# Optimization experiments

Measured on AMD Instinct MI355X. Metric: run time of the kernel, lower is better.

Reference implementation:

```python
import jax, jax.numpy as jnp
import numpy as np

N = 50000      # nodes
E = 800000     # edges (before self-loops)
NFEAT = 128
NHID = 32
H = 8
NCLASS = 47
NEG_SLOPE = 0.2  # PyG GATv2Conv default


def gatv2_layer(x, src, dst, Wl, Wr, att, b, n):
    """One GATv2Conv layer (concat over heads). att: [H, C]."""
    h, c = att.shape
    xl = (x @ Wl).reshape(n, h, c)  # source transform (lin_l)
    xr = (x @ Wr).reshape(n, h, c)  # target transform (lin_r)
    e = jax.nn.leaky_relu(xl[src] + xr[dst], NEG_SLOPE)   # [E, H, C]
    logits = jnp.einsum('ehc,hc->eh', e, att)             # [E, H]
    # segment softmax over incoming edges of each target node
    m = jax.ops.segment_max(logits, dst, num_segments=n)  # [N, H]
    alpha = jnp.exp(logits - m[dst])
    denom = jax.ops.segment_sum(alpha, dst, num_segments=n)
    alpha = alpha / (denom[dst] + 1e-16)
    msg = xl[src] * alpha[:, :, None]                     # [E, H, C]
    out = jax.ops.segment_sum(msg, dst, num_segments=n)   # [N, H, C]
    return out.reshape(n, h * c) + b


def setup_inputs():
    key = jax.random.key(0)
    ks = jax.random.split(key, 16)
    s = 0.1
    x = jax.random.normal(ks[0], (N, NFEAT), jnp.float32)
    edge_index = jax.random.randint(ks[1], (2, E), 0, N)
    HID = H * NHID  # 256
    params = dict(
        Wl0=jax.random.normal(ks[2], (NFEAT, HID), jnp.float32) * s,
        Wr0=jax.random.normal(ks[3], (NFEAT, HID), jnp.float32) * s,
        a0=jax.random.normal(ks[4], (H, NHID), jnp.float32) * s,
        b0=jnp.zeros((HID,), jnp.float32),
        Wl1=jax.random.normal(ks[5], (HID, HID), jnp.float32) * s,
        Wr1=jax.random.normal(ks[6], (HID, HID), jnp.float32) * s,
        a1=jax.random.normal(ks[7], (H, NHID), jnp.float32) * s,
        b1=jnp.zeros((HID,), jnp.float32),
        Wl2=jax.random.normal(ks[8], (HID, NCLASS), jnp.float32) * s,
        Wr2=jax.random.normal(ks[9], (HID, NCLASS), jnp.float32) * s,
        a2=jax.random.normal(ks[10], (1, NCLASS), jnp.float32) * s,
        b2=jnp.zeros((NCLASS,), jnp.float32),
    )
    return {"x": x, "edge_index": edge_index, **params}


def reference(x, edge_index, Wl0, Wr0, a0, b0, Wl1, Wr1, a1, b1, Wl2, Wr2, a2, b2):
    n = x.shape[0]
    # PyG GATv2Conv adds self-loops by default
    loops = jnp.arange(n, dtype=edge_index.dtype)
    src = jnp.concatenate([edge_index[0], loops])
    dst = jnp.concatenate([edge_index[1], loops])
    h = gatv2_layer(x, src, dst, Wl0, Wr0, a0, b0, n)
    h = jax.nn.elu(h)
    h = gatv2_layer(h, src, dst, Wl1, Wr1, a1, b1, n)
    h = jax.nn.elu(h)
    h = gatv2_layer(h, src, dst, Wl2, Wr2, a2, b2, n)
    return jax.nn.log_softmax(h, axis=-1)
```

## Files before the change

### kernel.cpp

```cpp
#include <hip/hip_runtime.h>
#include <cmath>


#define NFEAT 128
#define HID 256
#define NCLS 47
#define L2PAD 64

typedef __attribute__((ext_vector_type(8))) short bf16x8;
typedef __attribute__((ext_vector_type(4))) float f32x4;

__device__ __forceinline__ unsigned short f2b(float f) {
  unsigned int u = __builtin_bit_cast(unsigned int, f);
  u += 0x7FFFu + ((u >> 16) & 1u);
  return (unsigned short)(u >> 16);
}
__device__ __forceinline__ float b2f(unsigned short s) {
  return __builtin_bit_cast(float, (unsigned int)s << 16);
}
__device__ __forceinline__ float b2f_lo(unsigned int u) {
  return __builtin_bit_cast(float, u << 16);
}
__device__ __forceinline__ float b2f_hi(unsigned int u) {
  return __builtin_bit_cast(float, u & 0xFFFF0000u);
}

__device__ __forceinline__ float group8_sum(float v) {
  v += __shfl_xor(v, 1, 64);
  v += __shfl_xor(v, 2, 64);
  v += __shfl_xor(v, 4, 64);
  return v;
}

__global__ void k_cast_bf16(const float* __restrict__ in,
                            unsigned short* __restrict__ out, int n4) {
  int i = blockIdx.x * blockDim.x + threadIdx.x;
  if (i < n4) {
    float4 v = reinterpret_cast<const float4*>(in)[i];
    ushort4 o = {f2b(v.x), f2b(v.y), f2b(v.z), f2b(v.w)};
    reinterpret_cast<ushort4*>(out)[i] = o;
  }
}

__global__ void k_wt(const float* __restrict__ W, unsigned short* __restrict__ WT,
                     int K, int M, int Mpad) {
  int i = blockIdx.x * blockDim.x + threadIdx.x;
  if (i >= Mpad * K) return;
  int m = i / K, k = i - m * K;
  WT[i] = (m < M) ? f2b(W[(size_t)k * M + m]) : 0;
}

__global__ void k_init_deg(int* __restrict__ deg, int n) {
  int i = blockIdx.x * blockDim.x + threadIdx.x;
  if (i < n) deg[i] = 1;
}

__global__ void k_count(const int* __restrict__ dst, int* __restrict__ deg, int e) {
  int i = blockIdx.x * blockDim.x + threadIdx.x;
  if (i < e) atomicAdd(&deg[dst[i]], 1);
}

__global__ __launch_bounds__(256) void k_bsum(const int* __restrict__ deg,
                                              int* __restrict__ bsum, int n) {
  int t = threadIdx.x;
  int base = blockIdx.x * 1024 + t * 4;
  int s = 0;
  if (base + 3 < n) {
    int4 v = *reinterpret_cast<const int4*>(deg + base);
    s = v.x + v.y + v.z + v.w;
  } else {
    for (int j = 0; j < 4; ++j) { int i = base + j; if (i < n) s += deg[i]; }
  }
  #pragma unroll
  for (int off = 1; off < 64; off <<= 1) s += __shfl_xor(s, off, 64);
  __shared__ int wsum[4];
  if ((t & 63) == 0) wsum[t >> 6] = s;
  __syncthreads();
  if (t == 0) bsum[blockIdx.x] = wsum[0] + wsum[1] + wsum[2] + wsum[3];
}

__global__ void k_scanb(int* __restrict__ bsum, int nb) {
  int lane = threadIdx.x;
  int v = (lane < nb) ? bsum[lane] : 0;
  #pragma unroll
  for (int off = 1; off < 64; off <<= 1) {
    int u = __shfl_up(v, off, 64);
    if (lane >= off) v += u;
  }
  if (lane < nb) bsum[lane] = v;
}

__global__ __launch_bounds__(256) void k_scanfinal(const int* __restrict__ deg,
                                                   const int* __restrict__ bscan,
                                                   int* __restrict__ rowptr, int n) {
  int t = threadIdx.x, b = blockIdx.x;
  int base = b * 1024 + t * 4;
  int v0 = 0, v1 = 0, v2 = 0, v3 = 0;
  if (base + 3 < n) {
    int4 v = *reinterpret_cast<const int4*>(deg + base);
    v0 = v.x; v1 = v.y; v2 = v.z; v3 = v.w;
  } else {
    if (base < n) v0 = deg[base];
    if (base + 1 < n) v1 = deg[base + 1];
    if (base + 2 < n) v2 = deg[base + 2];
    if (base + 3 < n) v3 = deg[base + 3];
  }
  int s = v0 + v1 + v2 + v3;
  int incl = s;
  #pragma unroll
  for (int off = 1; off < 64; off <<= 1) {
    int u = __shfl_up(incl, off, 64);
    if ((t & 63) >= off) incl += u;
  }
  __shared__ int wsum[4];
  int w = t >> 6, l = t & 63;
  if (l == 63) wsum[w] = incl;
  __syncthreads();
  int woff = 0;
  for (int j = 0; j < w; ++j) woff += wsum[j];
  int excl = incl - s + woff;
  int boff = (b == 0) ? 0 : bscan[b - 1];
  int p = boff + excl;
  if (base < n)     rowptr[base + 1] = p + v0;
  if (base + 1 < n) rowptr[base + 2] = p + v0 + v1;
  if (base + 2 < n) rowptr[base + 3] = p + v0 + v1 + v2;
  if (base + 3 < n) rowptr[base + 4] = p + v0 + v1 + v2 + v3;
  if (b == 0 && t == 0) rowptr[0] = 0;
}

__global__ void k_init_csr(const int* __restrict__ rowptr, int* __restrict__ adj,
                           int* __restrict__ cursor, int n) {
  int i = blockIdx.x * blockDim.x + threadIdx.x;
  if (i < n) { int p = rowptr[i]; adj[p] = i; cursor[i] = p + 1; }
}

__global__ void k_scatter(const int* __restrict__ src, const int* __restrict__ dst,
                          int* __restrict__ cursor, int* __restrict__ adj, int e) {
  int i = blockIdx.x * blockDim.x + threadIdx.x;
  if (i < e) { int p = atomicAdd(&cursor[dst[i]], 1); adj[p] = src[i]; }
}

__global__ __launch_bounds__(256) void gemm_dual_bf16(
    const unsigned short* __restrict__ X, const unsigned short* __restrict__ WlT,
    const unsigned short* __restrict__ WrT, unsigned short* __restrict__ XL,
    unsigned short* __restrict__ XR, int N, int K, int Mpad) {
  __shared__ __align__(16) unsigned short Xs[64][72];
  __shared__ __align__(16) unsigned short Ls[64][72];
  __shared__ __align__(16) unsigned short Rs[64][72];

  const int t = threadIdx.x;
  const int row0 = blockIdx.x * 64;
  const int col0 = blockIdx.y * 64;
  const int w = t >> 6, lane = t & 63;
  const int r15 = lane & 15, kc = lane >> 4;

  f32x4 accL[4], accR[4];
  #pragma unroll
  for (int i = 0; i < 4; ++i) {
    accL[i] = (f32x4){0.f, 0.f, 0.f, 0.f};
    accR[i] = (f32x4){0.f, 0.f, 0.f, 0.f};
  }

  for (int k0 = 0; k0 < K; k0 += 64) {
    #pragma unroll
    for (int cc = 0; cc < 2; ++cc) {
      int c = t + cc * 256;
      int row = c >> 3, seg = (c & 7) * 8;
      int grow = row0 + row;
      if (grow < N) {
        *reinterpret_cast<uint4*>(&Xs[row][seg]) =
            *reinterpret_cast<const uint4*>(X + (size_t)grow * K + k0 + seg);
      } else {
        *reinterpret_cast<uint4*>(&Xs[row][seg]) = (uint4){0, 0, 0, 0};
      }
      *reinterpret_cast<uint4*>(&Ls[row][seg]) =
          *reinterpret_cast<const uint4*>(WlT + (size_t)(col0 + row) * K + k0 + seg);
      *reinterpret_cast<uint4*>(&Rs[row][seg]) =
          *reinterpret_cast<const uint4*>(WrT + (size_t)(col0 + row) * K + k0 + seg);
    }
    __syncthreads();

    #pragma unroll
    for (int ks = 0; ks < 2; ++ks) {
      const bf16x8 a = *reinterpret_cast<const bf16x8*>(&Xs[16 * w + r15][ks * 32 + kc * 8]);
      #pragma unroll
      for (int nf = 0; nf < 4; ++nf) {
        const bf16x8 bl = *reinterpret_cast<const bf16x8*>(&Ls[nf * 16 + r15][ks * 32 + kc * 8]);
        const bf16x8 br = *reinterpret_cast<const bf16x8*>(&Rs[nf * 16 + r15][ks * 32 + kc * 8]);
        accL[nf] = __builtin_amdgcn_mfma_f32_16x16x32_bf16(a, bl, accL[nf], 0, 0, 0);
        accR[nf] = __builtin_amdgcn_mfma_f32_16x16x32_bf16(a, br, accR[nf], 0, 0, 0);
      }
    }
    __syncthreads();
  }

  #pragma unroll
  for (int nf = 0; nf < 4; ++nf) {
    int cc = col0 + nf * 16 + r15;
    #pragma unroll
    for (int i = 0; i < 4; ++i) {
      int rr = row0 + 16 * w + kc * 4 + i;
      if (rr < N) {
        XL[(size_t)rr * Mpad + cc] = f2b(accL[nf][i]);
        XR[(size_t)rr * Mpad + cc] = f2b(accR[nf][i]);
      }
    }
  }
}

__global__ __launch_bounds__(256) void gat_node_hc(
    const unsigned short* __restrict__ xl, const unsigned short* __restrict__ xr,
    const float* __restrict__ att, const float* __restrict__ bias,
    const int* __restrict__ rowptr, const int* __restrict__ adj,
    unsigned short* __restrict__ out, int n) {
  int wid = (blockIdx.x * blockDim.x + threadIdx.x) >> 6;
  int lane = threadIdx.x & 63;
  if (wid >= n) return;

  uint2 pr = *reinterpret_cast<const uint2*>(xr + (size_t)wid * HID + lane * 4);
  const float xr0 = b2f_lo(pr.x), xr1 = b2f_hi(pr.x);
  const float xr2 = b2f_lo(pr.y), xr3 = b2f_hi(pr.y);
  const float4 a = *reinterpret_cast<const float4*>(att + lane * 4);

  float m = -INFINITY, denom = 0.f;
  float a0 = 0.f, a1 = 0.f, a2 = 0.f, a3 = 0.f;

#define EDGE_PREP(p, x0, x1, x2, x3, part)                                 \
  x0 = b2f_lo(p.x); x1 = b2f_hi(p.x); x2 = b2f_lo(p.y); x3 = b2f_hi(p.y);  \
  {                                                                        \
    float t0 = x0 + xr0, t1 = x1 + xr1, t2 = x2 + xr2, t3 = x3 + xr3;      \
    t0 = fmaxf(t0, 0.2f * t0); t1 = fmaxf(t1, 0.2f * t1);                  \
    t2 = fmaxf(t2, 0.2f * t2); t3 = fmaxf(t3, 0.2f * t3);                  \
    part = t0 * a.x + t1 * a.y + t2 * a.z + t3 * a.w;                      \
    part = group8_sum(part);                                               \
  }

#define SLOW_UPDATE(part, x0, x1, x2, x3)                                  \
  {                                                                        \
    float mn = fmaxf(m, part);                                             \
    float so = __expf(m - mn);                                             \
    float wn = __expf(part - mn);                                          \
    denom = denom * so + wn;                                               \
    a0 = a0 * so + wn * x0; a1 = a1 * so + wn * x1;                        \
    a2 = a2 * so + wn * x2; a3 = a3 * so + wn * x3;                        \
    m = mn;                                                                \
  }

  const int beg = rowptr[wid], end = rowptr[wid + 1];
  int i = beg;
  for (; i + 1 < end; i += 2) {
    int u0 = adj[i], u1 = adj[i + 1];
    uint2 p0 = *reinterpret_cast<const uint2*>(xl + (size_t)u0 * HID + lane * 4);
    uint2 p1 = *reinterpret_cast<const uint2*>(xl + (size_t)u1 * HID + lane * 4);
    float x00, x01, x02, x03, part0;
    float x10, x11, x12, x13, part1;
    EDGE_PREP(p0, x00, x01, x02, x03, part0);
    EDGE_PREP(p1, x10, x11, x12, x13, part1);
    float mx = fmaxf(part0, part1);
    if (__any(mx > m + 8.f)) {
      SLOW_UPDATE(part0, x00, x01, x02, x03);
      SLOW_UPDATE(part1, x10, x11, x12, x13);
    } else {
      float w0 = __expf(part0 - m), w1 = __expf(part1 - m);
      denom += w0 + w1;
      a0 += w0 * x00 + w1 * x10; a1 += w0 * x01 + w1 * x11;
      a2 += w0 * x02 + w1 * x12; a3 += w0 * x03 + w1 * x13;
    }
  }
  if (i < end) {
    int u0 = adj[i];
    uint2 p0 = *reinterpret_cast<const uint2*>(xl + (size_t)u0 * HID + lane * 4);
    float x00, x01, x02, x03, part0;
    EDGE_PREP(p0, x00, x01, x02, x03, part0);
    if (__any(part0 > m + 8.f)) {
      SLOW_UPDATE(part0, x00, x01, x02, x03);
    } else {
      float w0 = __expf(part0 - m);
      denom += w0;
      a0 += w0 * x00; a1 += w0 * x01; a2 += w0 * x02; a3 += w0 * x03;
    }
  }
#undef EDGE_PREP
#undef SLOW_UPDATE

  const float inv = 1.f / (denom + 1e-16f);
  const float4 bv = *reinterpret_cast<const float4*>(bias + lane * 4);
  float o[4] = {a0 * inv + bv.x, a1 * inv + bv.y, a2 * inv + bv.z, a3 * inv + bv.w};
  #pragma unroll
  for (int j = 0; j < 4; ++j) o[j] = o[j] > 0.f ? o[j] : (__expf(o[j]) - 1.f);
  ushort4 ov = {f2b(o[0]), f2b(o[1]), f2b(o[2]), f2b(o[3])};
  *reinterpret_cast<ushort4*>(out + (size_t)wid * HID + lane * 4) = ov;
}

__global__ __launch_bounds__(256) void gat_node_l2(
    const unsigned short* __restrict__ xl, const unsigned short* __restrict__ xr,
    const float* __restrict__ att, const float* __restrict__ bias,
    const int* __restrict__ rowptr, const int* __restrict__ adj,
    float* __restrict__ out, int n) {
  int wid = (blockIdx.x * blockDim.x + threadIdx.x) >> 6;
  int lane = threadIdx.x & 63;
  if (wid >= n) return;
  const bool act = lane < NCLS;

  const float xrv = act ? b2f(xr[(size_t)wid * L2PAD + lane]) : 0.f;
  const float a = act ? att[lane] : 0.f;

  float m = -INFINITY, denom = 0.f, acc = 0.f;

#define L2_PREP(u, xv, part)                                               \
  xv = act ? b2f(xl[(size_t)(u) * L2PAD + lane]) : 0.f;                    \
  {                                                                        \
    float e = xv + xrv; e = fmaxf(e, 0.2f * e);                            \
    part = e * a;                                                          \
    _Pragma("unroll")                                                      \
    for (int off = 1; off < 64; off <<= 1) part += __shfl_xor(part, off, 64); \
  }

#define L2_SLOW(part, xv)                                                  \
  {                                                                        \
    float mn = fmaxf(m, part);                                             \
    float so = __expf(m - mn);                                             \
    float wn = __expf(part - mn);                                          \
    denom = denom * so + wn;                                               \
    acc = acc * so + wn * xv;                                              \
    m = mn;                                                                \
  }

  const int beg = rowptr[wid], end = rowptr[wid + 1];
  int i = beg;
  for (; i + 1 < end; i += 2) {
    int u0 = adj[i], u1 = adj[i + 1];
    float xv0, part0, xv1, part1;
    L2_PREP(u0, xv0, part0);
    L2_PREP(u1, xv1, part1);
    float mx = fmaxf(part0, part1);
    if (mx > m + 8.f) {
      L2_SLOW(part0, xv0);
      L2_SLOW(part1, xv1);
    } else {
      float w0 = __expf(part0 - m), w1 = __expf(part1 - m);
      denom += w0 + w1;
      acc += w0 * xv0 + w1 * xv1;
    }
  }
  if (i < end) {
    int u0 = adj[i];
    float xv0, part0;
    L2_PREP(u0, xv0, part0);
    if (part0 > m + 8.f) {
      L2_SLOW(part0, xv0);
    } else {
      float w0 = __expf(part0 - m);
      denom += w0;
      acc += w0 * xv0;
    }
  }
#undef L2_PREP
#undef L2_SLOW

  float r = acc / (denom + 1e-16f) + (act ? bias[lane] : 0.f);
  float rm = act ? r : -INFINITY;
  #pragma unroll
  for (int off = 1; off < 64; off <<= 1) rm = fmaxf(rm, __shfl_xor(rm, off, 64));
  float se = act ? __expf(r - rm) : 0.f;
  #pragma unroll
  for (int off = 1; off < 64; off <<= 1) se += __shfl_xor(se, off, 64);
  if (act) out[(size_t)wid * NCLS + lane] = r - rm - __logf(se);
}

extern "C" void kernel_launch(void* const* d_in, const int* in_sizes, int n_in,
                              void* d_out, int out_size, void* d_ws, size_t ws_size,
                              hipStream_t stream) {
  const float* x   = (const float*)d_in[0];
  const int* ei    = (const int*)d_in[1];
  const float* Wl0 = (const float*)d_in[2];
  const float* Wr0 = (const float*)d_in[3];
  const float* a0  = (const float*)d_in[4];
  const float* b0  = (const float*)d_in[5];
  const float* Wl1 = (const float*)d_in[6];
  const float* Wr1 = (const float*)d_in[7];
  const float* a1  = (const float*)d_in[8];
  const float* b1  = (const float*)d_in[9];
  const float* Wl2 = (const float*)d_in[10];
  const float* Wr2 = (const float*)d_in[11];
  const float* a2  = (const float*)d_in[12];
  const float* b2  = (const float*)d_in[13];

  const int N = in_sizes[0] / NFEAT;
  const int E = in_sizes[1] / 2;
  const int* src = ei;
  const int* dst = ei + E;

  char* ws = (char*)d_ws;
  unsigned short* xlb = (unsigned short*)ws; ws += (size_t)N * HID * 2;
  unsigned short* xrb = (unsigned short*)ws; ws += (size_t)N * HID * 2;
  unsigned short* xb  = (unsigned short*)ws; ws += (size_t)N * NFEAT * 2;
  unsigned short* hb  = (unsigned short*)ws; ws += (size_t)N * HID * 2;
  unsigned short* hb2 = (unsigned short*)ws; ws += (size_t)N * HID * 2;
  unsigned short* WT  = (unsigned short*)ws; ws += (size_t)6 * HID * HID * 2;
  int* deg    = (int*)ws; ws += (size_t)N * sizeof(int);
  int* rowptr = (int*)ws; ws += (size_t)(N + 8) * sizeof(int);
  int* bsum   = (int*)ws; ws += (size_t)64 * sizeof(int);
  int* adj    = (int*)ws; ws += (size_t)(E + N) * sizeof(int);

  unsigned short* WlT0 = WT + 0 * HID * HID;
  unsigned short* WrT0 = WT + 1 * HID * HID;
  unsigned short* WlT1 = WT + 2 * HID * HID;
  unsigned short* WrT1 = WT + 3 * HID * HID;
  unsigned short* WlT2 = WT + 4 * HID * HID;
  unsigned short* WrT2 = WT + 5 * HID * HID;

  const int TB = 256;
  const int nbScan = (N + 1023) / 1024;

  k_cast_bf16<<<(N * NFEAT / 4 + TB - 1) / TB, TB, 0, stream>>>(x, xb, N * NFEAT / 4);
  k_wt<<<(HID * NFEAT + TB - 1) / TB, TB, 0, stream>>>(Wl0, WlT0, NFEAT, HID, HID);
  k_wt<<<(HID * NFEAT + TB - 1) / TB, TB, 0, stream>>>(Wr0, WrT0, NFEAT, HID, HID);
  k_wt<<<(HID * HID + TB - 1) / TB, TB, 0, stream>>>(Wl1, WlT1, HID, HID, HID);
  k_wt<<<(HID * HID + TB - 1) / TB, TB, 0, stream>>>(Wr1, WrT1, HID, HID, HID);
  k_wt<<<(L2PAD * HID + TB - 1) / TB, TB, 0, stream>>>(Wl2, WlT2, HID, NCLS, L2PAD);
  k_wt<<<(L2PAD * HID + TB - 1) / TB, TB, 0, stream>>>(Wr2, WrT2, HID, NCLS, L2PAD);

  k_init_deg<<<(N + TB - 1) / TB, TB, 0, stream>>>(deg, N);
  k_count<<<(E + TB - 1) / TB, TB, 0, stream>>>(dst, deg, E);
  k_bsum<<<nbScan, TB, 0, stream>>>(deg, bsum, N);
  k_scanb<<<1, 64, 0, stream>>>(bsum, nbScan);
  k_scanfinal<<<nbScan, TB, 0, stream>>>(deg, bsum, rowptr, N);
  k_init_csr<<<(N + TB - 1) / TB, TB, 0, stream>>>(rowptr, adj, deg, N);
  k_scatter<<<(E + TB - 1) / TB, TB, 0, stream>>>(src, dst, deg, adj, E);

  const int nodeBlocks = (N + 3) / 4;
  const int rowBlocks = (N + 63) / 64;

  {
    dim3 g(rowBlocks, HID / 64);
    gemm_dual_bf16<<<g, 256, 0, stream>>>(xb, WlT0, WrT0, xlb, xrb, N, NFEAT, HID);
    gat_node_hc<<<nodeBlocks, 256, 0, stream>>>(xlb, xrb, a0, b0, rowptr, adj, hb, N);
  }
  {
    dim3 g(rowBlocks, HID / 64);
    gemm_dual_bf16<<<g, 256, 0, stream>>>(hb, WlT1, WrT1, xlb, xrb, N, HID, HID);
    gat_node_hc<<<nodeBlocks, 256, 0, stream>>>(xlb, xrb, a1, b1, rowptr, adj, hb2, N);
  }
  {
    dim3 g(rowBlocks, 1);
    gemm_dual_bf16<<<g, 256, 0, stream>>>(hb2, WlT2, WrT2, xlb, xrb, N, HID, L2PAD);
    gat_node_l2<<<nodeBlocks, 256, 0, stream>>>(xlb, xrb, a2, b2, rowptr, adj,
                                                (float*)d_out, N);
  }
}
```

Baseline: 451.0 us.

## Split wave across two edges per step and precompute layer-2 edge logits

The hidden-layer aggregation kernel now has each wave's two 32-lane halves process different edges, each loading 8 bf16 features per lane. It keeps per-half online-softmax state and merges the halves at the end, which halves the shuffle-reduction depth and doubles the bytes per load. For the output layer, a new per-edge kernel computes all attention logits up front using a stored destination array. The node kernel then takes a plain max and does exp-weighted sums without per-edge 64-lane reductions. This costs extra work in CSR construction (a vdst array) plus an additional logit buffer pass, and it reuses xb as the layer-2 input buffer.

```diff
diff --git a/kernel.cpp b/kernel.cpp
--- a/kernel.cpp
+++ b/kernel.cpp
@@ -9,6 +9,7 @@
 
 typedef __attribute__((ext_vector_type(8))) short bf16x8;
 typedef __attribute__((ext_vector_type(4))) float f32x4;
+typedef __attribute__((ext_vector_type(2))) float f32x2;
 
 __device__ __forceinline__ unsigned short f2b(float f) {
   unsigned int u = __builtin_bit_cast(unsigned int, f);
@@ -18,18 +19,9 @@
 __device__ __forceinline__ float b2f(unsigned short s) {
   return __builtin_bit_cast(float, (unsigned int)s << 16);
 }
-__device__ __forceinline__ float b2f_lo(unsigned int u) {
-  return __builtin_bit_cast(float, u << 16);
-}
-__device__ __forceinline__ float b2f_hi(unsigned int u) {
-  return __builtin_bit_cast(float, u & 0xFFFF0000u);
-}
-
-__device__ __forceinline__ float group8_sum(float v) {
-  v += __shfl_xor(v, 1, 64);
-  v += __shfl_xor(v, 2, 64);
-  v += __shfl_xor(v, 4, 64);
-  return v;
+__device__ __forceinline__ f32x2 b2f2(unsigned int u) {
+  return (f32x2){__builtin_bit_cast(float, u << 16),
+                 __builtin_bit_cast(float, u & 0xFFFF0000u)};
 }
 
 __global__ void k_cast_bf16(const float* __restrict__ in,
@@ -48,6 +40,11 @@
   if (i >= Mpad * K) return;
   int m = i / K, k = i - m * K;
   WT[i] = (m < M) ? f2b(W[(size_t)k * M + m]) : 0;
+}
+
+__global__ void k_pad_att(const float* __restrict__ a, float* __restrict__ out48) {
+  int i = threadIdx.x;
+  if (i < 48) out48[i] = (i < NCLS) ? a[i] : 0.f;
 }
 
 __global__ void k_init_deg(int* __restrict__ deg, int n) {
@@ -129,15 +126,21 @@
 }
 
 __global__ void k_init_csr(const int* __restrict__ rowptr, int* __restrict__ adj,
-                           int* __restrict__ cursor, int n) {
-  int i = blockIdx.x * blockDim.x + threadIdx.x;
-  if (i < n) { int p = rowptr[i]; adj[p] = i; cursor[i] = p + 1; }
+                           int* __restrict__ vdst, int* __restrict__ cursor, int n) {
+  int i = blockIdx.x * blockDim.x + threadIdx.x;
+  if (i < n) { int p = rowptr[i]; adj[p] = i; vdst[p] = i; cursor[i] = p + 1; }
 }
 
 __global__ void k_scatter(const int* __restrict__ src, const int* __restrict__ dst,
-                          int* __restrict__ cursor, int* __restrict__ adj, int e) {
-  int i = blockIdx.x * blockDim.x + threadIdx.x;
-  if (i < e) { int p = atomicAdd(&cursor[dst[i]], 1); adj[p] = src[i]; }
+                          int* __restrict__ cursor, int* __restrict__ adj,
+                          int* __restrict__ vdst, int e) {
+  int i = blockIdx.x * blockDim.x + threadIdx.x;
+  if (i < e) {
+    int d = dst[i];
+    int p = atomicAdd(&cursor[d], 1);
+    adj[p] = src[i];
+    vdst[p] = d;
+  }
 }
 
 __global__ __launch_bounds__(256) void gemm_dual_bf16(
@@ -216,150 +219,147 @@
   int wid = (blockIdx.x * blockDim.x + threadIdx.x) >> 6;
   int lane = threadIdx.x & 63;
   if (wid >= n) return;
-
-  uint2 pr = *reinterpret_cast<const uint2*>(xr + (size_t)wid * HID + lane * 4);
-  const float xr0 = b2f_lo(pr.x), xr1 = b2f_hi(pr.x);
-  const float xr2 = b2f_lo(pr.y), xr3 = b2f_hi(pr.y);
-  const float4 a = *reinterpret_cast<const float4*>(att + lane * 4);
-
-  float m = -INFINITY, denom = 0.f;
-  float a0 = 0.f, a1 = 0.f, a2 = 0.f, a3 = 0.f;
-
-#define EDGE_PREP(p, x0, x1, x2, x3, part)                                 \
-  x0 = b2f_lo(p.x); x1 = b2f_hi(p.x); x2 = b2f_lo(p.y); x3 = b2f_hi(p.y);  \
-  {                                                                        \
-    float t0 = x0 + xr0, t1 = x1 + xr1, t2 = x2 + xr2, t3 = x3 + xr3;      \
-    t0 = fmaxf(t0, 0.2f * t0); t1 = fmaxf(t1, 0.2f * t1);                  \
-    t2 = fmaxf(t2, 0.2f * t2); t3 = fmaxf(t3, 0.2f * t3);                  \
-    part = t0 * a.x + t1 * a.y + t2 * a.z + t3 * a.w;                      \
-    part = group8_sum(part);                                               \
-  }
-
-#define SLOW_UPDATE(part, x0, x1, x2, x3)                                  \
-  {                                                                        \
-    float mn = fmaxf(m, part);                                             \
-    float so = __expf(m - mn);                                             \
-    float wn = __expf(part - mn);                                          \
-    denom = denom * so + wn;                                               \
-    a0 = a0 * so + wn * x0; a1 = a1 * so + wn * x1;                        \
-    a2 = a2 * so + wn * x2; a3 = a3 * so + wn * x3;                        \
-    m = mn;                                                                \
-  }
+  const int q = lane & 31, half = lane >> 5;
+
+  const uint4 xrp = *reinterpret_cast<const uint4*>(xr + (size_t)wid * HID + q * 8);
+  const f32x2 xr2[4] = {b2f2(xrp.x), b2f2(xrp.y), b2f2(xrp.z), b2f2(xrp.w)};
+  const float4 af0 = *reinterpret_cast<const float4*>(att + q * 8);
+  const float4 af1 = *reinterpret_cast<const float4*>(att + q * 8 + 4);
+  const f32x2 a2[4] = {{af0.x, af0.y}, {af0.z, af0.w},
+                       {af1.x, af1.y}, {af1.z, af1.w}};
+
+  float m = -1e30f, denom = 0.f;
+  f32x2 acc[4] = {{0.f, 0.f}, {0.f, 0.f}, {0.f, 0.f}, {0.f, 0.f}};
 
   const int beg = rowptr[wid], end = rowptr[wid + 1];
-  int i = beg;
-  for (; i + 1 < end; i += 2) {
-    int u0 = adj[i], u1 = adj[i + 1];
-    uint2 p0 = *reinterpret_cast<const uint2*>(xl + (size_t)u0 * HID + lane * 4);
-    uint2 p1 = *reinterpret_cast<const uint2*>(xl + (size_t)u1 * HID + lane * 4);
-    float x00, x01, x02, x03, part0;
-    float x10, x11, x12, x13, part1;
-    EDGE_PREP(p0, x00, x01, x02, x03, part0);
-    EDGE_PREP(p1, x10, x11, x12, x13, part1);
-    float mx = fmaxf(part0, part1);
-    if (__any(mx > m + 8.f)) {
-      SLOW_UPDATE(part0, x00, x01, x02, x03);
-      SLOW_UPDATE(part1, x10, x11, x12, x13);
+  for (int base = beg; base < end; base += 2) {
+    const int i = base + half;
+    const bool act = i < end;
+    const int u = adj[act ? i : base];
+    const uint4 p = *reinterpret_cast<const uint4*>(xl + (size_t)u * HID + q * 8);
+    const f32x2 x2[4] = {b2f2(p.x), b2f2(p.y), b2f2(p.z), b2f2(p.w)};
+    f32x2 s2 = x2[0] * 0.f;
+    #pragma unroll
+    for (int j = 0; j < 4; ++j) {
+      f32x2 z = x2[j] + xr2[j];
+      f32x2 lz = 0.2f * z;
+      f32x2 r = {fmaxf(z.x, lz.x), fmaxf(z.y, lz.y)};
+      s2 += r * a2[j];
+    }
+    float part = s2.x + s2.y;
+    part += __shfl_xor(part, 1, 64);
+    part += __shfl_xor(part, 2, 64);
+    if (!act) part = -1e30f;
+    if (__any(part > m + 8.f)) {
+      float mn = fmaxf(m, part);
+      float so = __expf(m - mn);
+      float wn = act ? __expf(part - mn) : 0.f;
+      denom = denom * so + wn;
+      #pragma unroll
+      for (int j = 0; j < 4; ++j) acc[j] = acc[j] * so + wn * x2[j];
+      m = mn;
     } else {
-      float w0 = __expf(part0 - m), w1 = __expf(part1 - m);
-      denom += w0 + w1;
-      a0 += w0 * x00 + w1 * x10; a1 += w0 * x01 + w1 * x11;
-      a2 += w0 * x02 + w1 * x12; a3 += w0 * x03 + w1 * x13;
-    }
-  }
-  if (i < end) {
-    int u0 = adj[i];
-    uint2 p0 = *reinterpret_cast<const uint2*>(xl + (size_t)u0 * HID + lane * 4);
-    float x00, x01, x02, x03, part0;
-    EDGE_PREP(p0, x00, x01, x02, x03, part0);
-    if (__any(part0 > m + 8.f)) {
-      SLOW_UPDATE(part0, x00, x01, x02, x03);
-    } else {
-      float w0 = __expf(part0 - m);
-      denom += w0;
-      a0 += w0 * x00; a1 += w0 * x01; a2 += w0 * x02; a3 += w0 * x03;
-    }
-  }
-#undef EDGE_PREP
-#undef SLOW_UPDATE
-
-  const float inv = 1.f / (denom + 1e-16f);
-  const float4 bv = *reinterpret_cast<const float4*>(bias + lane * 4);
-  float o[4] = {a0 * inv + bv.x, a1 * inv + bv.y, a2 * inv + bv.z, a3 * inv + bv.w};
-  #pragma unroll
-  for (int j = 0; j < 4; ++j) o[j] = o[j] > 0.f ? o[j] : (__expf(o[j]) - 1.f);
-  ushort4 ov = {f2b(o[0]), f2b(o[1]), f2b(o[2]), f2b(o[3])};
-  *reinterpret_cast<ushort4*>(out + (size_t)wid * HID + lane * 4) = ov;
+      float wn = act ? __expf(part - m) : 0.f;
+      denom += wn;
+      #pragma unroll
+      for (int j = 0; j < 4; ++j) acc[j] += wn * x2[j];
+    }
+  }
+
+  float mo = __shfl_xor(m, 32, 64);
+  float ms = fmaxf(m, mo);
+  float sc = __expf(m - ms);
+  denom *= sc;
+  denom += __shfl_xor(denom, 32, 64);
+  #pragma unroll
+  for (int j = 0; j < 4; ++j) {
+    acc[j] *= sc;
+    acc[j].x += __shfl_xor(acc[j].x, 32, 64);
+    acc[j].y += __shfl_xor(acc[j].y, 32, 64);
+  }
+
+  if (half == 0) {
+    const float inv = 1.f / (denom + 1e-16f);
+    const float4 bf0 = *reinterpret_cast<const float4*>(bias + q * 8);
+    const float4 bf1 = *reinterpret_cast<const float4*>(bias + q * 8 + 4);
+    float o[8] = {acc[0].x * inv + bf0.x, acc[0].y * inv + bf0.y,
+                  acc[1].x * inv + bf0.z, acc[1].y * inv + bf0.w,
+                  acc[2].x * inv + bf1.x, acc[2].y * inv + bf1.y,
+                  acc[3].x * inv + bf1.z, acc[3].y * inv + bf1.w};
+    #pragma unroll
+    for (int j = 0; j < 8; ++j) o[j] = o[j] > 0.f ? o[j] : (__expf(o[j]) - 1.f);
+    uint4 ov;
+    ov.x = (unsigned)f2b(o[0]) | ((unsigned)f2b(o[1]) << 16);
+    ov.y = (unsigned)f2b(o[2]) | ((unsigned)f2b(o[3]) << 16);
+    ov.z = (unsigned)f2b(o[4]) | ((unsigned)f2b(o[5]) << 16);
+    ov.w = (unsigned)f2b(o[6]) | ((unsigned)f2b(o[7]) << 16);
+    *reinterpret_cast<uint4*>(out + (size_t)wid * HID + q * 8) = ov;
+  }
+}
+
+__global__ __launch_bounds__(256) void k_logit_l2(
+    const unsigned short* __restrict__ xl, const unsigned short* __restrict__ xr,
+    const float* __restrict__ att48, const int* __restrict__ adj,
+    const int* __restrict__ vdst, float* __restrict__ logit, int total) {
+  int i = blockIdx.x * blockDim.x + threadIdx.x;
+  if (i >= total) return;
+  const int u = adj[i], v = vdst[i];
+  const uint4* pu = reinterpret_cast<const uint4*>(xl + (size_t)u * L2PAD);
+  const uint4* pv = reinterpret_cast<const uint4*>(xr + (size_t)v * L2PAD);
+  f32x2 s2 = {0.f, 0.f};
+  #pragma unroll
+  for (int b = 0; b < 6; ++b) {
+    const uint4 xu = pu[b], xv = pv[b];
+    const f32x2* a2 = reinterpret_cast<const f32x2*>(att48 + b * 8);
+    const unsigned ua[4] = {xu.x, xu.y, xu.z, xu.w};
+    const unsigned va[4] = {xv.x, xv.y, xv.z, xv.w};
+    #pragma unroll
+    for (int j = 0; j < 4; ++j) {
+      f32x2 z = b2f2(ua[j]) + b2f2(va[j]);
+      f32x2 lz = 0.2f * z;
+      f32x2 r = {fmaxf(z.x, lz.x), fmaxf(z.y, lz.y)};
+      s2 += r * a2[j];
+    }
+  }
+  logit[i] = s2.x + s2.y;
 }
 
 __global__ __launch_bounds__(256) void gat_node_l2(
-    const unsigned short* __restrict__ xl, const unsigned short* __restrict__ xr,
-    const float* __restrict__ att, const float* __restrict__ bias,
-    const int* __restrict__ rowptr, const int* __restrict__ adj,
-    float* __restrict__ out, int n) {
+    const unsigned short* __restrict__ xl, const float* __restrict__ logit,
+    const float* __restrict__ bias, const int* __restrict__ rowptr,
+    const int* __restrict__ adj, float* __restrict__ out, int n) {
   int wid = (blockIdx.x * blockDim.x + threadIdx.x) >> 6;
   int lane = threadIdx.x & 63;
   if (wid >= n) return;
   const bool act = lane < NCLS;
-
-  const float xrv = act ? b2f(xr[(size_t)wid * L2PAD + lane]) : 0.f;
-  const float a = act ? att[lane] : 0.f;
-
-  float m = -INFINITY, denom = 0.f, acc = 0.f;
-
-#define L2_PREP(u, xv, part)                                               \
-  xv = act ? b2f(xl[(size_t)(u) * L2PAD + lane]) : 0.f;                    \
-  {                                                                        \
-    float e = xv + xrv; e = fmaxf(e, 0.2f * e);                            \
-    part = e * a;                                                          \
-    _Pragma("unroll")                                                      \
-    for (int off = 1; off < 64; off <<= 1) part += __shfl_xor(part, off, 64); \
-  }
-
-#define L2_SLOW(part, xv)                                                  \
-  {                                                                        \
-    float mn = fmaxf(m, part);                                             \
-    float so = __expf(m - mn);                                             \
-    float wn = __expf(part - mn);                                          \
-    denom = denom * so + wn;                                               \
-    acc = acc * so + wn * xv;                                              \
-    m = mn;                                                                \
-  }
-
   const int beg = rowptr[wid], end = rowptr[wid + 1];
+
+  float mx = -1e30f;
+  for (int i = beg + lane; i < end; i += 64) mx = fmaxf(mx, logit[i]);
+  #pragma unroll
+  for (int off = 1; off < 64; off <<= 1) mx = fmaxf(mx, __shfl_xor(mx, off, 64));
+
+  float denom = 0.f, acc = 0.f;
   int i = beg;
   for (; i + 1 < end; i += 2) {
     int u0 = adj[i], u1 = adj[i + 1];
-    float xv0, part0, xv1, part1;
-    L2_PREP(u0, xv0, part0);
-    L2_PREP(u1, xv1, part1);
-    float mx = fmaxf(part0, part1);
-    if (mx > m + 8.f) {
-      L2_SLOW(part0, xv0);
-      L2_SLOW(part1, xv1);
-    } else {
-      float w0 = __expf(part0 - m), w1 = __expf(part1 - m);
-      denom += w0 + w1;
-      acc += w0 * xv0 + w1 * xv1;
-    }
+    float w0 = __expf(logit[i] - mx);
+    float w1 = __expf(logit[i + 1] - mx);
+    float x0 = act ? b2f(xl[(size_t)u0 * L2PAD + lane]) : 0.f;
+    float x1 = act ? b2f(xl[(size_t)u1 * L2PAD + lane]) : 0.f;
+    denom += w0 + w1;
+    acc += w0 * x0 + w1 * x1;
   }
   if (i < end) {
     int u0 = adj[i];
-    float xv0, part0;
-    L2_PREP(u0, xv0, part0);
-    if (part0 > m + 8.f) {
-      L2_SLOW(part0, xv0);
-    } else {
-      float w0 = __expf(part0 - m);
-      denom += w0;
-      acc += w0 * xv0;
-    }
-  }
-#undef L2_PREP
-#undef L2_SLOW
+    float w0 = __expf(logit[i] - mx);
+    float x0 = act ? b2f(xl[(size_t)u0 * L2PAD + lane]) : 0.f;
+    denom += w0;
+    acc += w0 * x0;
+  }
 
   float r = acc / (denom + 1e-16f) + (act ? bias[lane] : 0.f);
-  float rm = act ? r : -INFINITY;
+  float rm = act ? r : -1e30f;
   #pragma unroll
   for (int off = 1; off < 64; off <<= 1) rm = fmaxf(rm, __shfl_xor(rm, off, 64));
   float se = act ? __expf(r - rm) : 0.f;
@@ -390,18 +390,21 @@
   const int E = in_sizes[1] / 2;
   const int* src = ei;
   const int* dst = ei + E;
+  const int total = E + N;
 
   char* ws = (char*)d_ws;
   unsigned short* xlb = (unsigned short*)ws; ws += (size_t)N * HID * 2;
   unsigned short* xrb = (unsigned short*)ws; ws += (size_t)N * HID * 2;
-  unsigned short* xb  = (unsigned short*)ws; ws += (size_t)N * NFEAT * 2;
+  unsigned short* xb  = (unsigned short*)ws; ws += (size_t)N * HID * 2;
   unsigned short* hb  = (unsigned short*)ws; ws += (size_t)N * HID * 2;
-  unsigned short* hb2 = (unsigned short*)ws; ws += (size_t)N * HID * 2;
   unsigned short* WT  = (unsigned short*)ws; ws += (size_t)6 * HID * HID * 2;
+  float* logit = (float*)ws; ws += (size_t)total * sizeof(float);
+  float* att48 = (float*)ws; ws += 64 * sizeof(float);
   int* deg    = (int*)ws; ws += (size_t)N * sizeof(int);
   int* rowptr = (int*)ws; ws += (size_t)(N + 8) * sizeof(int);
   int* bsum   = (int*)ws; ws += (size_t)64 * sizeof(int);
-  int* adj    = (int*)ws; ws += (size_t)(E + N) * sizeof(int);
+  int* adj    = (int*)ws; ws += (size_t)total * sizeof(int);
+  int* vdst   = (int*)ws; ws += (size_t)total * sizeof(int);
 
   unsigned short* WlT0 = WT + 0 * HID * HID;
   unsigned short* WrT0 = WT + 1 * HID * HID;
@@ -420,14 +423,15 @@
   k_wt<<<(HID * HID + TB - 1) / TB, TB, 0, stream>>>(Wr1, WrT1, HID, HID, HID);
   k_wt<<<(L2PAD * HID + TB - 1) / TB, TB, 0, stream>>>(Wl2, WlT2, HID, NCLS, L2PAD);
   k_wt<<<(L2PAD * HID + TB - 1) / TB, TB, 0, stream>>>(Wr2, WrT2, HID, NCLS, L2PAD);
+  k_pad_att<<<1, 64, 0, stream>>>(a2, att48);
 
   k_init_deg<<<(N + TB - 1) / TB, TB, 0, stream>>>(deg, N);
   k_count<<<(E + TB - 1) / TB, TB, 0, stream>>>(dst, deg, E);
   k_bsum<<<nbScan, TB, 0, stream>>>(deg, bsum, N);
   k_scanb<<<1, 64, 0, stream>>>(bsum, nbScan);
   k_scanfinal<<<nbScan, TB, 0, stream>>>(deg, bsum, rowptr, N);
-  k_init_csr<<<(N + TB - 1) / TB, TB, 0, stream>>>(rowptr, adj, deg, N);
-  k_scatter<<<(E + TB - 1) / TB, TB, 0, stream>>>(src, dst, deg, adj, E);
+  k_init_csr<<<(N + TB - 1) / TB, TB, 0, stream>>>(rowptr, adj, vdst, deg, N);
+  k_scatter<<<(E + TB - 1) / TB, TB, 0, stream>>>(src, dst, deg, adj, vdst, E);
 
   const int nodeBlocks = (N + 3) / 4;
   const int rowBlocks = (N + 63) / 64;
@@ -440,12 +444,14 @@
   {
     dim3 g(rowBlocks, HID / 64);
     gemm_dual_bf16<<<g, 256, 0, stream>>>(hb, WlT1, WrT1, xlb, xrb, N, HID, HID);
-    gat_node_hc<<<nodeBlocks, 256, 0, stream>>>(xlb, xrb, a1, b1, rowptr, adj, hb2, N);
+    gat_node_hc<<<nodeBlocks, 256, 0, stream>>>(xlb, xrb, a1, b1, rowptr, adj, xb, N);
   }
   {
     dim3 g(rowBlocks, 1);
-    gemm_dual_bf16<<<g, 256, 0, stream>>>(hb2, WlT2, WrT2, xlb, xrb, N, HID, L2PAD);
-    gat_node_l2<<<nodeBlocks, 256, 0, stream>>>(xlb, xrb, a2, b2, rowptr, adj,
+    gemm_dual_bf16<<<g, 256, 0, stream>>>(xb, WlT2, WrT2, xlb, xrb, N, HID, L2PAD);
+    k_logit_l2<<<(total + TB - 1) / TB, TB, 0, stream>>>(xlb, xrb, att48, adj,
+                                                         vdst, logit, total);
+    gat_node_l2<<<nodeBlocks, 256, 0, stream>>>(xlb, logit, b2, rowptr, adj,
                                                 (float*)d_out, N);
   }
 }
```

Result: no change. 445.1 us (-1.3%).
